# Kernel tuning notes

Measured on AMD Instinct MI355X. Metric: run time of the kernel, lower is better.

Reference implementation:

```python
import jax, jax.numpy as jnp
import numpy as np


def _pano_affinity():
    # Faithful port of get_pano_affinity(): 3 rings of 12 views, 3x3 Gaussian
    # blur (cv2 ksize=3 sigma=0 => sigma=0.8), BORDER_TRANSPARENT (borders kept),
    # diagonal reset to 1; zeros replaced by 0.01 as done in __init__.
    p = np.eye(36, dtype=np.float64)
    for v in range(12):  # top ring
        p[v, v + 12] = 1
        l = (v - 1) % 12
        r = (v + 1) % 12
        p[v, l] = 1; p[v, l + 12] = 1
        p[v, r] = 1; p[v, r + 12] = 1
    for v in range(12, 24):  # middle ring
        p[v, v + 12] = 1; p[v, v - 12] = 1
        l = (v - 13) % 12 + 12
        r = (v - 11) % 12 + 12
        p[v, l] = 1; p[v, l + 12] = 1; p[v, l - 12] = 1
        p[v, r] = 1; p[v, r + 12] = 1; p[v, r - 12] = 1
    for v in range(24, 36):  # bottom ring
        p[v, v - 12] = 1
        l = (v - 25) % 12 + 24
        r = (v - 23) % 12 + 24
        p[v, l] = 1; p[v, l - 12] = 1
        p[v, r] = 1; p[v, r - 12] = 1
    assert np.sum(p - p.T) == 0
    kern = np.exp(-np.array([-1.0, 0.0, 1.0]) ** 2 / (2 * 0.8 ** 2))
    kern /= kern.sum()
    a, b = kern[0], kern[1]
    t = a * p[:, :-2] + b * p[:, 1:-1] + a * p[:, 2:]
    t2 = a * t[:-2, :] + b * t[1:-1, :] + a * t[2:, :]
    out = p.copy()
    out[1:-1, 1:-1] = t2  # transparent border: edge pixels unblurred
    out[np.eye(36, dtype=bool)] = 1.0
    out[out == 0] = 0.01
    return out.astype(np.float32)


def _ln(x, g, b):
    mu = jnp.mean(x, -1, keepdims=True)
    v = jnp.mean(jnp.square(x - mu), -1, keepdims=True)
    return (x - mu) * jax.lax.rsqrt(v + 1e-5) * g + b


def setup_inputs() -> dict:
    key = jax.random.key(0)
    ks = jax.random.split(key, 12)
    B, L, V, D, KD, KV, Q, H = 128, 36, 36, 512, 300, 112, 36, 512
    s = 0.02
    return {
        'h': jax.random.normal(ks[0], (B, Q), jnp.float32),
        'context': jax.random.normal(ks[1], (B, L, V, D), jnp.float32),
        'teacher_action_view_ids': jax.random.randint(ks[2], (B,), 0, 36),
        'detect_feats': jax.random.normal(ks[3], (B, L, KD), jnp.float32),
        'knowledge_vector': jax.random.normal(ks[4], (B, L, KV), jnp.float32),
        'pano_a': jnp.asarray(_pano_affinity()),
        'W_q': jax.random.normal(ks[5], (Q, Q), jnp.float32) * s,
        'W_k': jax.random.normal(ks[6], (Q, D + KD), jnp.float32) * s,
        'gru_Wih': jax.random.normal(ks[7], (3 * Q, D + KV), jnp.float32) * s,
        'gru_Whh': jax.random.normal(ks[8], (3 * Q, Q), jnp.float32) * s,
        'gru_bih': jnp.zeros((3 * Q,), jnp.float32),
        'gru_bhh': jnp.zeros((3 * Q,), jnp.float32),
        'ln_slots_g': jnp.ones((Q,), jnp.float32),
        'ln_slots_b': jnp.zeros((Q,), jnp.float32),
        'ln_ff_g': jnp.ones((Q,), jnp.float32),
        'ln_ff_b': jnp.zeros((Q,), jnp.float32),
        'mlp_W1': jax.random.normal(ks[9], (H, Q), jnp.float32) * s,
        'mlp_b1': jnp.zeros((H,), jnp.float32),
        'mlp_W2': jax.random.normal(ks[10], (Q, H), jnp.float32) * s,
        'mlp_b2': jnp.zeros((Q,), jnp.float32),
    }


def reference(h, context, teacher_action_view_ids, detect_feats, knowledge_vector,
              pano_a, W_q, W_k, gru_Wih, gru_Whh, gru_bih, gru_bhh,
              ln_slots_g, ln_slots_b, ln_ff_g, ln_ff_b,
              mlp_W1, mlp_b1, mlp_W2, mlp_b2):
    B, L, V, D = context.shape
    Q = pano_a.shape[0]  # 36
    scale = Q ** -0.5
    iters = 3
    slots = jnp.broadcast_to(pano_a, (B, Q, Q))
    # context_know = cat(context, detect_feats broadcast over 36 views)
    ck = jnp.concatenate(
        [context, jnp.broadcast_to(detect_feats[:, :, None, :], (B, L, V, detect_feats.shape[-1]))], axis=-1)
    k = jnp.einsum('bljc,qc->bljq', ck, W_k)  # [B,L,36,Q]
    attn_ws = []
    for _ in range(iters):
        slots_prev = slots
        q = jnp.einsum('bie,qe->biq', _ln(slots, ln_slots_g, ln_slots_b), W_q)  # [B,Q,Q]
        dots = jnp.einsum('bid,bkjd->bkj', q, k) * scale  # i summed out, as in source
        attn = jax.nn.softmax(dots, axis=-1)  # softmax over views
        attn_ws.append(attn)
        updates = jnp.einsum('bkjd,bij->bid', context, attn)  # [B,L,D]
        x = jnp.concatenate([updates, knowledge_vector], axis=-1).reshape(-1, D + knowledge_vector.shape[-1])
        hp = slots_prev.reshape(-1, Q)
        # torch.nn.GRUCell (gate order r, z, n)
        gx = x @ gru_Wih.T + gru_bih
        gh = hp @ gru_Whh.T + gru_bhh
        xr, xz, xn = jnp.split(gx, 3, axis=-1)
        hr, hz, hn = jnp.split(gh, 3, axis=-1)
        r = jax.nn.sigmoid(xr + hr)
        z = jax.nn.sigmoid(xz + hz)
        n = jnp.tanh(xn + r * hn)
        gnew = ((1.0 - z) * n + z * hp).reshape(B, -1, Q)
        ff = _ln(gnew, ln_ff_g, ln_ff_b)
        gnew = gnew + (jax.nn.relu(ff @ mlp_W1.T + mlp_b1) @ mlp_W2.T + mlp_b2)
        slots = gnew
    return slots, jnp.stack(attn_ws, 0)
```

## Files before the change

### kernel.cpp

```cpp
#include <hip/hip_runtime.h>

namespace {
constexpr int Bc = 128, Lc = 36, Vc = 36, Dc = 512, KDc = 300, KVc = 112, Qc = 36, Hc = 512;
constexpr int ROWS = Bc * Lc * Vc;
constexpr int BLn  = Bc * Lc;
constexpr int SLOT = Bc * Qc * Qc;
constexpr float SCALE = 1.0f / 6.0f;
}

__device__ __forceinline__ float wave_sum(float v) {
  #pragma unroll
  for (int off = 32; off > 0; off >>= 1) v += __shfl_xor(v, off, 64);
  return v;
}
__device__ __forceinline__ float wave_max(float v) {
  #pragma unroll
  for (int off = 32; off > 0; off >>= 1) v = fmaxf(v, __shfl_xor(v, off, 64));
  return v;
}
__device__ __forceinline__ float sigmoidf_(float x) { return 1.f / (1.f + __expf(-x)); }

__global__ void init_slots_kernel(const float* __restrict__ pano, float* __restrict__ slots) {
  int idx = blockIdx.x * 256 + threadIdx.x;
  slots[idx] = pano[idx % (Qc * Qc)];
}

__global__ __launch_bounds__(256) void csum_kernel(const float* __restrict__ ctx, float* __restrict__ csum) {
  int tid = blockIdx.x * 256 + threadIdx.x;
  int b  = tid / (Vc * Dc);
  int jd = tid % (Vc * Dc);
  const float* p = ctx + (size_t)b * Lc * Vc * Dc + jd;
  float s = 0.f;
  #pragma unroll
  for (int l = 0; l < Lc; ++l) s += p[(size_t)l * (Vc * Dc)];
  csum[tid] = s;
}

__global__ void kd_kernel(const float* __restrict__ det, const float* __restrict__ Wk,
                          float* __restrict__ kd) {
  __shared__ float ds[KDc];
  int bl = blockIdx.x; int t = threadIdx.x;
  for (int c = t; c < KDc; c += 64) ds[c] = det[(size_t)bl * KDc + c];
  __syncthreads();
  if (t < Qc) {
    const float* w = Wk + (size_t)t * 812 + 512;
    float acc = 0.f;
    #pragma unroll 4
    for (int c = 0; c < KDc; ++c) acc = fmaf(ds[c], w[c], acc);
    kd[(size_t)bl * Qc + t] = acc;
  }
}

__global__ __launch_bounds__(256) void k_gemm(const float* __restrict__ A, const float* __restrict__ Wk,
                       const float* __restrict__ kd, float* __restrict__ kout) {
  __shared__ __align__(16) float As[32 * 260];
  __shared__ __align__(16) float Bs[32 * 48];
  int t = threadIdx.x;
  int rb = blockIdx.x * 256;
  int tr = t & 63, tc = t >> 6;
  float acc[4][9];
  #pragma unroll
  for (int i = 0; i < 4; ++i)
    #pragma unroll
    for (int c = 0; c < 9; ++c) acc[i][c] = 0.f;

  for (int d0 = 0; d0 < 512; d0 += 32) {
    #pragma unroll
    for (int jj = 0; jj < 8; ++jj) {
      int idx = t + jj * 256;
      int kkb = (idx & 7) * 4, r = idx >> 3;
      const float4 v = *(const float4*)(A + (size_t)(rb + r) * 512 + d0 + kkb);
      As[(kkb + 0) * 260 + r] = v.x;
      As[(kkb + 1) * 260 + r] = v.y;
      As[(kkb + 2) * 260 + r] = v.z;
      As[(kkb + 3) * 260 + r] = v.w;
    }
    for (int idx = t; idx < 32 * 36; idx += 256) {
      int kk = idx / 36, c = idx % 36;
      Bs[kk * 48 + (c / 9) * 12 + (c % 9)] = Wk[(size_t)c * 812 + d0 + kk];
    }
    __syncthreads();
    #pragma unroll
    for (int kk = 0; kk < 32; ++kk) {
      const float4 a  = *(const float4*)&As[kk * 260 + tr * 4];
      const float* bp = &Bs[kk * 48 + tc * 12];
      const float4 b0 = *(const float4*)bp;
      const float4 b1 = *(const float4*)(bp + 4);
      const float  b8 = bp[8];
      const float av[4] = {a.x, a.y, a.z, a.w};
      const float bv[9] = {b0.x, b0.y, b0.z, b0.w, b1.x, b1.y, b1.z, b1.w, b8};
      #pragma unroll
      for (int i = 0; i < 4; ++i)
        #pragma unroll
        for (int c = 0; c < 9; ++c) acc[i][c] = fmaf(av[i], bv[c], acc[i][c]);
    }
    __syncthreads();
  }
  #pragma unroll
  for (int i = 0; i < 4; ++i) {
    int row = rb + tr * 4 + i;
    int bl = row / 36;
    #pragma unroll
    for (int c = 0; c < 9; ++c) {
      int q = tc * 9 + c;
      kout[(size_t)row * 36 + q] = acc[i][c] + kd[(size_t)bl * 36 + q];
    }
  }
}

__global__ __launch_bounds__(256) void prew_gemm(const float* __restrict__ A, int lda, int K, int k0,
                                                 const float* __restrict__ Wih, float* __restrict__ outp) {
  __shared__ __align__(16) float As[16 * 68];
  __shared__ __align__(16) float Bs[16 * 112];
  int t = threadIdx.x;
  int rb = blockIdx.x * 64;
  int tr = t & 63, tc = t >> 6;
  float acc[27];
  #pragma unroll
  for (int c = 0; c < 27; ++c) acc[c] = 0.f;

  for (int kk0 = 0; kk0 < K; kk0 += 16) {
    {
      int r = t >> 2, kq = (t & 3) * 4;
      const float4 v = *(const float4*)(A + (size_t)(rb + r) * lda + kk0 + kq);
      As[(kq + 0) * 68 + r] = v.x;
      As[(kq + 1) * 68 + r] = v.y;
      As[(kq + 2) * 68 + r] = v.z;
      As[(kq + 3) * 68 + r] = v.w;
    }
    for (int idx = t; idx < 16 * 108; idx += 256) {
      int k = idx / 108, c = idx % 108;
      Bs[k * 112 + (c / 27) * 28 + (c % 27)] = Wih[(size_t)c * 624 + k0 + kk0 + k];
    }
    __syncthreads();
    #pragma unroll
    for (int k = 0; k < 16; ++k) {
      const float a = As[k * 68 + tr];
      const float* bp = &Bs[k * 112 + tc * 28];
      float bv[27];
      #pragma unroll
      for (int c4 = 0; c4 < 6; ++c4) {
        float4 b4 = *(const float4*)(bp + c4 * 4);
        bv[c4 * 4 + 0] = b4.x; bv[c4 * 4 + 1] = b4.y; bv[c4 * 4 + 2] = b4.z; bv[c4 * 4 + 3] = b4.w;
      }
      bv[24] = bp[24]; bv[25] = bp[25]; bv[26] = bp[26];
      #pragma unroll
      for (int c = 0; c < 27; ++c) acc[c] = fmaf(a, bv[c], acc[c]);
    }
    __syncthreads();
  }
  int row = rb + tr;
  #pragma unroll
  for (int c = 0; c < 27; ++c)
    outp[(size_t)row * 108 + tc * 27 + c] = acc[c];
}

__global__ void lnqsum_kernel(const float* __restrict__ slots, const float* __restrict__ Wq,
                              const float* __restrict__ g, const float* __restrict__ bb,
                              float* __restrict__ qsum) {
  int b = blockIdx.x, lane = threadIdx.x;
  __shared__ float ls[Qc];
  float gv = 0.f, bv = 0.f;
  if (lane < Qc) { gv = g[lane]; bv = bb[lane]; }
  float lnsum = 0.f;
  for (int i = 0; i < Qc; ++i) {
    float x = (lane < Qc) ? slots[((size_t)b * Qc + i) * Qc + lane] : 0.f;
    float mu = wave_sum(x) * (1.f / 36.f);
    float d = x - mu;
    float var = wave_sum((lane < Qc) ? d * d : 0.f) * (1.f / 36.f);
    float ln = d * rsqrtf(var + 1e-5f) * gv + bv;
    if (lane < Qc) lnsum += ln;
  }
  if (lane < Qc) ls[lane] = lnsum;
  __syncthreads();
  if (lane < Qc) {
    float acc = 0.f;
    #pragma unroll
    for (int e = 0; e < Qc; ++e) acc = fmaf(ls[e], Wq[lane * Qc + e], acc);
    qsum[(size_t)b * Qc + lane] = acc;
  }
}

__global__ void dots_kernel(const float* __restrict__ kmat, const float* __restrict__ qsum,
                            float* __restrict__ attn_out) {
  int bl = blockIdx.x;
  int b = bl / Lc;
  int lane = threadIdx.x;
  __shared__ float qs[Qc];
  if (lane < Qc) qs[lane] = qsum[(size_t)b * Qc + lane];
  __syncthreads();
  float dot = 0.f;
  if (lane < Vc) {
    const float* kp = kmat + ((size_t)bl * Vc + lane) * Qc;
    #pragma unroll
    for (int c = 0; c < 9; ++c) {
      float4 kv = *(const float4*)(kp + c * 4);
      dot += kv.x * qs[4 * c] + kv.y * qs[4 * c + 1] + kv.z * qs[4 * c + 2] + kv.w * qs[4 * c + 3];
    }
  }
  dot *= SCALE;
  float m = wave_max((lane < Vc) ? dot : -1e30f);
  float e = (lane < Vc) ? __expf(dot - m) : 0.f;
  float s = wave_sum(e);
  if (lane < Vc) attn_out[(size_t)bl * Vc + lane] = e / s;
}

__global__ __launch_bounds__(128) void gxmix_kernel(const float* __restrict__ attn, const float* __restrict__ cw,
                             const float* __restrict__ gknw, float* __restrict__ gx) {
  int b = blockIdx.x;
  int c = threadIdx.x;
  __shared__ float at[Qc * Vc];
  for (int idx = threadIdx.x; idx < Qc * Vc; idx += 128) at[idx] = attn[(size_t)b * Qc * Vc + idx];
  __syncthreads();
  if (c >= 108) return;
  float cwv[36];
  #pragma unroll
  for (int j = 0; j < 36; ++j) cwv[j] = cw[((size_t)b * 36 + j) * 108 + c];
  #pragma unroll 2
  for (int i = 0; i < 36; ++i) {
    float acc = gknw[((size_t)b * 36 + i) * 108 + c];
    #pragma unroll
    for (int j = 0; j < 36; ++j) acc = fmaf(at[i * 36 + j], cwv[j], acc);
    gx[((size_t)b * 36 + i) * 108 + c] = acc;
  }
}

__global__ void gate_kernel(const float* __restrict__ slots, const float* __restrict__ gx,
                            const float* __restrict__ Whh, const float* __restrict__ bih,
                            const float* __restrict__ bhh, const float* __restrict__ lng,
                            const float* __restrict__ lnb, const float* __restrict__ b2,
                            float* __restrict__ ff, float* __restrict__ snew) {
  int row = blockIdx.x, lane = threadIdx.x;
  __shared__ float hps[Qc];
  float hp = 0.f;
  if (lane < Qc) { hp = slots[(size_t)row * Qc + lane]; hps[lane] = hp; }
  __syncthreads();
  float hprime = 0.f;
  if (lane < Qc) {
    float hr = bhh[lane], hz = bhh[36 + lane], hn = bhh[72 + lane];
    #pragma unroll 4
    for (int e = 0; e < Qc; ++e) {
      float h = hps[e];
      hr = fmaf(h, Whh[lane * 36 + e], hr);
      hz = fmaf(h, Whh[(36 + lane) * 36 + e], hz);
      hn = fmaf(h, Whh[(72 + lane) * 36 + e], hn);
    }
    float xr = gx[(size_t)row * 108 + lane]      + bih[lane];
    float xz = gx[(size_t)row * 108 + 36 + lane] + bih[36 + lane];
    float xn = gx[(size_t)row * 108 + 72 + lane] + bih[72 + lane];
    float r = sigmoidf_(xr + hr);
    float z = sigmoidf_(xz + hz);
    float n = tanhf(xn + r * hn);
    hprime = (1.f - z) * n + z * hp;
  }
  float mu = wave_sum((lane < Qc) ? hprime : 0.f) * (1.f / 36.f);
  float dd = hprime - mu;
  float var = wave_sum((lane < Qc) ? dd * dd : 0.f) * (1.f / 36.f);
  float rstd = rsqrtf(var + 1e-5f);
  if (lane < Qc) {
    ff[(size_t)row * Qc + lane]   = dd * rstd * lng[lane] + lnb[lane];
    snew[(size_t)row * Qc + lane] = hprime + b2[lane];
  }
}

__global__ __launch_bounds__(256) void mlp1_kernel(const float* __restrict__ ff, const float* __restrict__ W1,
                         const float* __restrict__ b1, float* __restrict__ mid) {
  __shared__ __align__(16) float As[36 * 68];
  __shared__ __align__(16) float Bs[36 * 132];
  int t = threadIdx.x;
  int mt = blockIdx.x % 72, nt = blockIdx.x / 72;
  int rb = mt * 64, cb = nt * 128;
  for (int idx = t; idx < 64 * 36; idx += 256) {
    int r = idx / 36, e = idx % 36;
    As[e * 68 + r] = ff[(size_t)(rb + r) * 36 + e];
  }
  for (int idx = t; idx < 128 * 36; idx += 256) {
    int c = idx / 36, e = idx % 36;
    Bs[e * 132 + c] = W1[(size_t)(cb + c) * 36 + e];
  }
  __syncthreads();
  int tr = t & 31, tc = t >> 5;
  float acc[2][16];
  #pragma unroll
  for (int ri = 0; ri < 2; ++ri)
    #pragma unroll
    for (int c = 0; c < 16; ++c) acc[ri][c] = 0.f;
  #pragma unroll 4
  for (int e = 0; e < 36; ++e) {
    const float2 a = *(const float2*)&As[e * 68 + tr * 2];
    const float* bp = &Bs[e * 132 + tc * 16];
    float bv[16];
    #pragma unroll
    for (int c4 = 0; c4 < 4; ++c4) {
      float4 b4 = *(const float4*)(bp + c4 * 4);
      bv[c4 * 4 + 0] = b4.x; bv[c4 * 4 + 1] = b4.y; bv[c4 * 4 + 2] = b4.z; bv[c4 * 4 + 3] = b4.w;
    }
    #pragma unroll
    for (int c = 0; c < 16; ++c) {
      acc[0][c] = fmaf(a.x, bv[c], acc[0][c]);
      acc[1][c] = fmaf(a.y, bv[c], acc[1][c]);
    }
  }
  #pragma unroll
  for (int ri = 0; ri < 2; ++ri) {
    int row = rb + tr * 2 + ri;
    #pragma unroll
    for (int c4 = 0; c4 < 4; ++c4) {
      int c0 = cb + tc * 16 + c4 * 4;
      float4 o;
      o.x = fmaxf(acc[ri][c4 * 4 + 0] + b1[c0 + 0], 0.f);
      o.y = fmaxf(acc[ri][c4 * 4 + 1] + b1[c0 + 1], 0.f);
      o.z = fmaxf(acc[ri][c4 * 4 + 2] + b1[c0 + 2], 0.f);
      o.w = fmaxf(acc[ri][c4 * 4 + 3] + b1[c0 + 3], 0.f);
      *(float4*)&mid[(size_t)row * 512 + c0] = o;
    }
  }
}

__global__ __launch_bounds__(256) void mlp2_kernel(const float* __restrict__ mid, const float* __restrict__ W2,
                         float* __restrict__ snew) {
  __shared__ __align__(16) float As[32 * 68];
  __shared__ __align__(16) float Bs[32 * 48];
  int t = threadIdx.x;
  int rb = blockIdx.x * 64;
  int tr = t & 63, tc = t >> 6;
  float acc[9];
  #pragma unroll
  for (int c = 0; c < 9; ++c) acc[c] = 0.f;
  for (int d0 = 0; d0 < 512; d0 += 32) {
    #pragma unroll
    for (int jj = 0; jj < 2; ++jj) {
      int idx = t + jj * 256;
      int kkb = (idx & 7) * 4, r = idx >> 3;
      const float4 v = *(const float4*)(mid + (size_t)(rb + r) * 512 + d0 + kkb);
      As[(kkb + 0) * 68 + r] = v.x;
      As[(kkb + 1) * 68 + r] = v.y;
      As[(kkb + 2) * 68 + r] = v.z;
      As[(kkb + 3) * 68 + r] = v.w;
    }
    for (int idx = t; idx < 36 * 32; idx += 256) {
      int kk = idx / 36, c = idx % 36;
      Bs[kk * 48 + (c / 9) * 12 + (c % 9)] = W2[(size_t)c * 512 + d0 + kk];
    }
    __syncthreads();
    #pragma unroll
    for (int kk = 0; kk < 32; ++kk) {
      const float a = As[kk * 68 + tr];
      const float* bp = &Bs[kk * 48 + tc * 12];
      const float4 b0 = *(const float4*)bp;
      const float4 b1 = *(const float4*)(bp + 4);
      const float  b8 = bp[8];
      const float bv[9] = {b0.x, b0.y, b0.z, b0.w, b1.x, b1.y, b1.z, b1.w, b8};
      #pragma unroll
      for (int c = 0; c < 9; ++c) acc[c] = fmaf(a, bv[c], acc[c]);
    }
    __syncthreads();
  }
  int row = rb + tr;
  #pragma unroll
  for (int c = 0; c < 9; ++c) {
    size_t o = (size_t)row * 36 + tc * 9 + c;
    snew[o] = snew[o] + acc[c];
  }
}

__global__ void copy_kernel(const float* __restrict__ src, float* __restrict__ dst) {
  int idx = blockIdx.x * 256 + threadIdx.x;
  dst[idx] = src[idx];
}

extern "C" void kernel_launch(void* const* d_in, const int* in_sizes, int n_in,
                              void* d_out, int out_size, void* d_ws, size_t ws_size,
                              hipStream_t stream) {
  const float* ctx  = (const float*)d_in[1];
  const float* det  = (const float*)d_in[3];
  const float* knw  = (const float*)d_in[4];
  const float* pano = (const float*)d_in[5];
  const float* Wq   = (const float*)d_in[6];
  const float* Wk   = (const float*)d_in[7];
  const float* Wih  = (const float*)d_in[8];
  const float* Whh  = (const float*)d_in[9];
  const float* bih  = (const float*)d_in[10];
  const float* bhh  = (const float*)d_in[11];
  const float* lsg  = (const float*)d_in[12];
  const float* lsb  = (const float*)d_in[13];
  const float* lfg  = (const float*)d_in[14];
  const float* lfb  = (const float*)d_in[15];
  const float* W1   = (const float*)d_in[16];
  const float* b1   = (const float*)d_in[17];
  const float* W2   = (const float*)d_in[18];
  const float* b2   = (const float*)d_in[19];
  float* out = (float*)d_out;

  float* w = (float*)d_ws;
  float* kmat   = w; w += (size_t)ROWS * 36;
  float* csum   = w; w += (size_t)Bc * Vc * Dc;
  float* mid    = csum;
  float* kd     = w; w += (size_t)BLn * Qc;
  float* slotsA = w; w += SLOT;
  float* slotsB = w; w += SLOT;
  float* qsum   = w; w += Bc * Qc;
  float* cw     = w; w += (size_t)BLn * 108;
  float* gknw   = w; w += (size_t)BLn * 108;
  float* gx     = w; w += (size_t)BLn * 108;
  float* ffb    = w; w += SLOT;

  float* cur = slotsA;
  float* nxt = slotsB;

  init_slots_kernel<<<648, 256, 0, stream>>>(pano, cur);
  csum_kernel<<<(Bc * Vc * Dc) / 256, 256, 0, stream>>>(ctx, csum);
  kd_kernel<<<BLn, 64, 0, stream>>>(det, Wk, kd);
  k_gemm<<<ROWS / 256, 256, 0, stream>>>(ctx, Wk, kd, kmat);
  prew_gemm<<<72, 256, 0, stream>>>(csum, 512, 512, 0,   Wih, cw);
  prew_gemm<<<72, 256, 0, stream>>>(knw,  112, 112, 512, Wih, gknw);

  for (int it = 0; it < 3; ++it) {
    float* attn = out + SLOT + (size_t)it * SLOT;
    lnqsum_kernel<<<Bc, 64, 0, stream>>>(cur, Wq, lsg, lsb, qsum);
    dots_kernel<<<BLn, 64, 0, stream>>>(kmat, qsum, attn);
    gxmix_kernel<<<Bc, 128, 0, stream>>>(attn, cw, gknw, gx);
    gate_kernel<<<BLn, 64, 0, stream>>>(cur, gx, Whh, bih, bhh, lfg, lfb, b2, ffb, nxt);
    mlp1_kernel<<<72 * 4, 256, 0, stream>>>(ffb, W1, b1, mid);
    mlp2_kernel<<<72, 256, 0, stream>>>(mid, W2, nxt);
    float* tmp = cur; cur = nxt; nxt = tmp;
  }
  copy_kernel<<<SLOT / 256, 256, 0, stream>>>(cur, out);
}
```

Measured before the change: 1.163 ms.

## Fuse recurrent slot-attention iterations into one per-batch persistent kernel

```diff
diff --git a/kernel.cpp b/kernel.cpp
--- a/kernel.cpp
+++ b/kernel.cpp
@@ -19,11 +19,6 @@
   return v;
 }
 __device__ __forceinline__ float sigmoidf_(float x) { return 1.f / (1.f + __expf(-x)); }
-
-__global__ void init_slots_kernel(const float* __restrict__ pano, float* __restrict__ slots) {
-  int idx = blockIdx.x * 256 + threadIdx.x;
-  slots[idx] = pano[idx % (Qc * Qc)];
-}
 
 __global__ __launch_bounds__(256) void csum_kernel(const float* __restrict__ ctx, float* __restrict__ csum) {
   int tid = blockIdx.x * 256 + threadIdx.x;
@@ -155,218 +150,182 @@
     outp[(size_t)row * 108 + tc * 27 + c] = acc[c];
 }
 
-__global__ void lnqsum_kernel(const float* __restrict__ slots, const float* __restrict__ Wq,
-                              const float* __restrict__ g, const float* __restrict__ bb,
-                              float* __restrict__ qsum) {
-  int b = blockIdx.x, lane = threadIdx.x;
-  __shared__ float ls[Qc];
-  float gv = 0.f, bv = 0.f;
-  if (lane < Qc) { gv = g[lane]; bv = bb[lane]; }
-  float lnsum = 0.f;
-  for (int i = 0; i < Qc; ++i) {
-    float x = (lane < Qc) ? slots[((size_t)b * Qc + i) * Qc + lane] : 0.f;
-    float mu = wave_sum(x) * (1.f / 36.f);
-    float d = x - mu;
-    float var = wave_sum((lane < Qc) ? d * d : 0.f) * (1.f / 36.f);
-    float ln = d * rsqrtf(var + 1e-5f) * gv + bv;
-    if (lane < Qc) lnsum += ln;
-  }
-  if (lane < Qc) ls[lane] = lnsum;
+__global__ __launch_bounds__(256) void mega_kernel(
+    const float* __restrict__ pano, const float* __restrict__ kmat,
+    const float* __restrict__ cw,   const float* __restrict__ gknw,
+    const float* __restrict__ Wq,   const float* __restrict__ Whh,
+    const float* __restrict__ bih,  const float* __restrict__ bhh,
+    const float* __restrict__ lsg,  const float* __restrict__ lsb,
+    const float* __restrict__ lfg,  const float* __restrict__ lfb,
+    const float* __restrict__ W1,   const float* __restrict__ b1,
+    const float* __restrict__ W2,   const float* __restrict__ b2,
+    float* __restrict__ out) {
+  const int b = blockIdx.x;
+  const int t = threadIdx.x;
+  const int wv = t >> 6, lane = t & 63;
+
+  __shared__ float s0[36 * 37], s1[36 * 37];
+  __shared__ float at[36 * 36];
+  __shared__ float cw_s[36 * 108], gk_s[36 * 108];
+  __shared__ float whh_s[108 * 37];
+  __shared__ float ff_s[36 * 37];
+  __shared__ float ls4[192];
+  __shared__ float qs[36];
+  __shared__ __align__(16) float wst[128 * 37];
+  __shared__ __align__(16) float mid_s[36 * 132];
+
+  for (int idx = t; idx < 1296; idx += 256) s0[(idx / 36) * 37 + idx % 36] = pano[idx];
+  for (int idx = t; idx < 3888; idx += 256) {
+    cw_s[idx] = cw[(size_t)b * 3888 + idx];
+    gk_s[idx] = gknw[(size_t)b * 3888 + idx];
+    whh_s[(idx / 36) * 37 + idx % 36] = Whh[idx];
+  }
+  float gv = 0.f, bv = 0.f, fg = 0.f, fb = 0.f, b2v = 0.f;
+  if (lane < 36) { gv = lsg[lane]; bv = lsb[lane]; fg = lfg[lane]; fb = lfb[lane]; b2v = b2[lane]; }
+  const float* kb = kmat + (size_t)b * 1296 * 36;
   __syncthreads();
-  if (lane < Qc) {
-    float acc = 0.f;
-    #pragma unroll
-    for (int e = 0; e < Qc; ++e) acc = fmaf(ls[e], Wq[lane * Qc + e], acc);
-    qsum[(size_t)b * Qc + lane] = acc;
-  }
-}
-
-__global__ void dots_kernel(const float* __restrict__ kmat, const float* __restrict__ qsum,
-                            float* __restrict__ attn_out) {
-  int bl = blockIdx.x;
-  int b = bl / Lc;
-  int lane = threadIdx.x;
-  __shared__ float qs[Qc];
-  if (lane < Qc) qs[lane] = qsum[(size_t)b * Qc + lane];
-  __syncthreads();
-  float dot = 0.f;
-  if (lane < Vc) {
-    const float* kp = kmat + ((size_t)bl * Vc + lane) * Qc;
-    #pragma unroll
-    for (int c = 0; c < 9; ++c) {
-      float4 kv = *(const float4*)(kp + c * 4);
-      dot += kv.x * qs[4 * c] + kv.y * qs[4 * c + 1] + kv.z * qs[4 * c + 2] + kv.w * qs[4 * c + 3];
-    }
-  }
-  dot *= SCALE;
-  float m = wave_max((lane < Vc) ? dot : -1e30f);
-  float e = (lane < Vc) ? __expf(dot - m) : 0.f;
-  float s = wave_sum(e);
-  if (lane < Vc) attn_out[(size_t)bl * Vc + lane] = e / s;
-}
-
-__global__ __launch_bounds__(128) void gxmix_kernel(const float* __restrict__ attn, const float* __restrict__ cw,
-                             const float* __restrict__ gknw, float* __restrict__ gx) {
-  int b = blockIdx.x;
-  int c = threadIdx.x;
-  __shared__ float at[Qc * Vc];
-  for (int idx = threadIdx.x; idx < Qc * Vc; idx += 128) at[idx] = attn[(size_t)b * Qc * Vc + idx];
-  __syncthreads();
-  if (c >= 108) return;
-  float cwv[36];
-  #pragma unroll
-  for (int j = 0; j < 36; ++j) cwv[j] = cw[((size_t)b * 36 + j) * 108 + c];
-  #pragma unroll 2
-  for (int i = 0; i < 36; ++i) {
-    float acc = gknw[((size_t)b * 36 + i) * 108 + c];
-    #pragma unroll
-    for (int j = 0; j < 36; ++j) acc = fmaf(at[i * 36 + j], cwv[j], acc);
-    gx[((size_t)b * 36 + i) * 108 + c] = acc;
-  }
-}
-
-__global__ void gate_kernel(const float* __restrict__ slots, const float* __restrict__ gx,
-                            const float* __restrict__ Whh, const float* __restrict__ bih,
-                            const float* __restrict__ bhh, const float* __restrict__ lng,
-                            const float* __restrict__ lnb, const float* __restrict__ b2,
-                            float* __restrict__ ff, float* __restrict__ snew) {
-  int row = blockIdx.x, lane = threadIdx.x;
-  __shared__ float hps[Qc];
-  float hp = 0.f;
-  if (lane < Qc) { hp = slots[(size_t)row * Qc + lane]; hps[lane] = hp; }
-  __syncthreads();
-  float hprime = 0.f;
-  if (lane < Qc) {
-    float hr = bhh[lane], hz = bhh[36 + lane], hn = bhh[72 + lane];
-    #pragma unroll 4
-    for (int e = 0; e < Qc; ++e) {
-      float h = hps[e];
-      hr = fmaf(h, Whh[lane * 36 + e], hr);
-      hz = fmaf(h, Whh[(36 + lane) * 36 + e], hz);
-      hn = fmaf(h, Whh[(72 + lane) * 36 + e], hn);
-    }
-    float xr = gx[(size_t)row * 108 + lane]      + bih[lane];
-    float xz = gx[(size_t)row * 108 + 36 + lane] + bih[36 + lane];
-    float xn = gx[(size_t)row * 108 + 72 + lane] + bih[72 + lane];
-    float r = sigmoidf_(xr + hr);
-    float z = sigmoidf_(xz + hz);
-    float n = tanhf(xn + r * hn);
-    hprime = (1.f - z) * n + z * hp;
-  }
-  float mu = wave_sum((lane < Qc) ? hprime : 0.f) * (1.f / 36.f);
-  float dd = hprime - mu;
-  float var = wave_sum((lane < Qc) ? dd * dd : 0.f) * (1.f / 36.f);
-  float rstd = rsqrtf(var + 1e-5f);
-  if (lane < Qc) {
-    ff[(size_t)row * Qc + lane]   = dd * rstd * lng[lane] + lnb[lane];
-    snew[(size_t)row * Qc + lane] = hprime + b2[lane];
-  }
-}
-
-__global__ __launch_bounds__(256) void mlp1_kernel(const float* __restrict__ ff, const float* __restrict__ W1,
-                         const float* __restrict__ b1, float* __restrict__ mid) {
-  __shared__ __align__(16) float As[36 * 68];
-  __shared__ __align__(16) float Bs[36 * 132];
-  int t = threadIdx.x;
-  int mt = blockIdx.x % 72, nt = blockIdx.x / 72;
-  int rb = mt * 64, cb = nt * 128;
-  for (int idx = t; idx < 64 * 36; idx += 256) {
-    int r = idx / 36, e = idx % 36;
-    As[e * 68 + r] = ff[(size_t)(rb + r) * 36 + e];
-  }
-  for (int idx = t; idx < 128 * 36; idx += 256) {
-    int c = idx / 36, e = idx % 36;
-    Bs[e * 132 + c] = W1[(size_t)(cb + c) * 36 + e];
-  }
-  __syncthreads();
-  int tr = t & 31, tc = t >> 5;
-  float acc[2][16];
-  #pragma unroll
-  for (int ri = 0; ri < 2; ++ri)
-    #pragma unroll
-    for (int c = 0; c < 16; ++c) acc[ri][c] = 0.f;
-  #pragma unroll 4
-  for (int e = 0; e < 36; ++e) {
-    const float2 a = *(const float2*)&As[e * 68 + tr * 2];
-    const float* bp = &Bs[e * 132 + tc * 16];
-    float bv[16];
-    #pragma unroll
-    for (int c4 = 0; c4 < 4; ++c4) {
-      float4 b4 = *(const float4*)(bp + c4 * 4);
-      bv[c4 * 4 + 0] = b4.x; bv[c4 * 4 + 1] = b4.y; bv[c4 * 4 + 2] = b4.z; bv[c4 * 4 + 3] = b4.w;
-    }
-    #pragma unroll
-    for (int c = 0; c < 16; ++c) {
-      acc[0][c] = fmaf(a.x, bv[c], acc[0][c]);
-      acc[1][c] = fmaf(a.y, bv[c], acc[1][c]);
-    }
-  }
-  #pragma unroll
-  for (int ri = 0; ri < 2; ++ri) {
-    int row = rb + tr * 2 + ri;
-    #pragma unroll
-    for (int c4 = 0; c4 < 4; ++c4) {
-      int c0 = cb + tc * 16 + c4 * 4;
-      float4 o;
-      o.x = fmaxf(acc[ri][c4 * 4 + 0] + b1[c0 + 0], 0.f);
-      o.y = fmaxf(acc[ri][c4 * 4 + 1] + b1[c0 + 1], 0.f);
-      o.z = fmaxf(acc[ri][c4 * 4 + 2] + b1[c0 + 2], 0.f);
-      o.w = fmaxf(acc[ri][c4 * 4 + 3] + b1[c0 + 3], 0.f);
-      *(float4*)&mid[(size_t)row * 512 + c0] = o;
-    }
-  }
-}
-
-__global__ __launch_bounds__(256) void mlp2_kernel(const float* __restrict__ mid, const float* __restrict__ W2,
-                         float* __restrict__ snew) {
-  __shared__ __align__(16) float As[32 * 68];
-  __shared__ __align__(16) float Bs[32 * 48];
-  int t = threadIdx.x;
-  int rb = blockIdx.x * 64;
-  int tr = t & 63, tc = t >> 6;
-  float acc[9];
-  #pragma unroll
-  for (int c = 0; c < 9; ++c) acc[c] = 0.f;
-  for (int d0 = 0; d0 < 512; d0 += 32) {
-    #pragma unroll
-    for (int jj = 0; jj < 2; ++jj) {
-      int idx = t + jj * 256;
-      int kkb = (idx & 7) * 4, r = idx >> 3;
-      const float4 v = *(const float4*)(mid + (size_t)(rb + r) * 512 + d0 + kkb);
-      As[(kkb + 0) * 68 + r] = v.x;
-      As[(kkb + 1) * 68 + r] = v.y;
-      As[(kkb + 2) * 68 + r] = v.z;
-      As[(kkb + 3) * 68 + r] = v.w;
-    }
-    for (int idx = t; idx < 36 * 32; idx += 256) {
-      int kk = idx / 36, c = idx % 36;
-      Bs[kk * 48 + (c / 9) * 12 + (c % 9)] = W2[(size_t)c * 512 + d0 + kk];
-    }
-    __syncthreads();
-    #pragma unroll
-    for (int kk = 0; kk < 32; ++kk) {
-      const float a = As[kk * 68 + tr];
-      const float* bp = &Bs[kk * 48 + tc * 12];
-      const float4 b0 = *(const float4*)bp;
-      const float4 b1 = *(const float4*)(bp + 4);
-      const float  b8 = bp[8];
-      const float bv[9] = {b0.x, b0.y, b0.z, b0.w, b1.x, b1.y, b1.z, b1.w, b8};
-      #pragma unroll
-      for (int c = 0; c < 9; ++c) acc[c] = fmaf(a, bv[c], acc[c]);
-    }
-    __syncthreads();
-  }
-  int row = rb + tr;
-  #pragma unroll
-  for (int c = 0; c < 9; ++c) {
-    size_t o = (size_t)row * 36 + tc * 9 + c;
-    snew[o] = snew[o] + acc[c];
-  }
-}
-
-__global__ void copy_kernel(const float* __restrict__ src, float* __restrict__ dst) {
-  int idx = blockIdx.x * 256 + threadIdx.x;
-  dst[idx] = src[idx];
+
+  #pragma unroll
+  for (int it = 0; it < 3; ++it) {
+    float* cur = (it == 1) ? s1 : s0;
+    float* nxt = (it == 1) ? s0 : s1;
+    float* aout = out + SLOT + (size_t)it * SLOT + (size_t)b * 1296;
+
+    float lnsum = 0.f;
+    #pragma unroll
+    for (int ii = 0; ii < 9; ++ii) {
+      int i = wv + 4 * ii;
+      float x = (lane < 36) ? cur[i * 37 + lane] : 0.f;
+      float mu = wave_sum(x) * (1.f / 36.f);
+      float d = x - mu;
+      float var = wave_sum((lane < 36) ? d * d : 0.f) * (1.f / 36.f);
+      float ln = d * rsqrtf(var + 1e-5f) * gv + bv;
+      if (lane < 36) lnsum += ln;
+    }
+    if (lane < 36) ls4[wv * 37 + lane] = lnsum;
+    __syncthreads();
+    if (t < 36) {
+      float l0 = ls4[t] + ls4[37 + t] + ls4[74 + t] + ls4[111 + t];
+      ls4[148 + t] = l0;
+    }
+    if (t < 36) {
+      float acc = 0.f;
+      #pragma unroll
+      for (int e = 0; e < 36; ++e) acc = fmaf(ls4[148 + e], Wq[t * 36 + e], acc);
+      qs[t] = acc;
+    }
+    __syncthreads();
+
+    #pragma unroll
+    for (int ii = 0; ii < 9; ++ii) {
+      int l = wv * 9 + ii;
+      float dot = 0.f;
+      if (lane < 36) {
+        const float* kp = kb + ((size_t)l * 36 + lane) * 36;
+        #pragma unroll
+        for (int c = 0; c < 9; ++c) {
+          float4 kv = *(const float4*)(kp + 4 * c);
+          dot += kv.x * qs[4 * c] + kv.y * qs[4 * c + 1] + kv.z * qs[4 * c + 2] + kv.w * qs[4 * c + 3];
+        }
+      }
+      dot *= SCALE;
+      float m = wave_max((lane < 36) ? dot : -1e30f);
+      float e = (lane < 36) ? __expf(dot - m) : 0.f;
+      float s = wave_sum(e);
+      if (lane < 36) {
+        float a = e / s;
+        at[l * 36 + lane] = a;
+        aout[(size_t)l * 36 + lane] = a;
+      }
+    }
+    __syncthreads();
+
+    for (int idx = t; idx < 1296; idx += 256) {
+      int i = idx / 36, c = idx % 36;
+      const float* ar = &at[i * 36];
+      float xr = gk_s[i * 108 + c]      + bih[c];
+      float xz = gk_s[i * 108 + 36 + c] + bih[36 + c];
+      float xn = gk_s[i * 108 + 72 + c] + bih[72 + c];
+      #pragma unroll 4
+      for (int j = 0; j < 36; ++j) {
+        float a = ar[j];
+        xr = fmaf(a, cw_s[j * 108 + c],      xr);
+        xz = fmaf(a, cw_s[j * 108 + 36 + c], xz);
+        xn = fmaf(a, cw_s[j * 108 + 72 + c], xn);
+      }
+      float hr = bhh[c], hz = bhh[36 + c], hn = bhh[72 + c];
+      const float* hrow = &cur[i * 37];
+      #pragma unroll 4
+      for (int e = 0; e < 36; ++e) {
+        float h = hrow[e];
+        hr = fmaf(h, whh_s[c * 37 + e],        hr);
+        hz = fmaf(h, whh_s[(36 + c) * 37 + e], hz);
+        hn = fmaf(h, whh_s[(72 + c) * 37 + e], hn);
+      }
+      float r = sigmoidf_(xr + hr), z = sigmoidf_(xz + hz);
+      float n = tanhf(xn + r * hn);
+      nxt[i * 37 + c] = (1.f - z) * n + z * hrow[c];
+    }
+    __syncthreads();
+
+    #pragma unroll
+    for (int ii = 0; ii < 9; ++ii) {
+      int i = wv * 9 + ii;
+      float v = (lane < 36) ? nxt[i * 37 + lane] : 0.f;
+      float mu = wave_sum(v) * (1.f / 36.f);
+      float d = v - mu;
+      float var = wave_sum((lane < 36) ? d * d : 0.f) * (1.f / 36.f);
+      float rstd = rsqrtf(var + 1e-5f);
+      if (lane < 36) {
+        ff_s[i * 37 + lane] = d * rstd * fg + fb;
+        nxt[i * 37 + lane] = v + b2v;
+      }
+    }
+    __syncthreads();
+
+    float acc[6] = {0.f, 0.f, 0.f, 0.f, 0.f, 0.f};
+    for (int h0 = 0; h0 < 512; h0 += 128) {
+      for (int idx = t; idx < 4608; idx += 256)
+        wst[(idx / 36) * 37 + idx % 36] = W1[(size_t)h0 * 36 + idx];
+      __syncthreads();
+      for (int idx = t; idx < 4608; idx += 256) {
+        int i = idx >> 7, hh = idx & 127;
+        float a = b1[h0 + hh];
+        const float* fr = &ff_s[i * 37];
+        const float* wr = &wst[hh * 37];
+        #pragma unroll 4
+        for (int e = 0; e < 36; ++e) a = fmaf(fr[e], wr[e], a);
+        mid_s[i * 132 + hh] = fmaxf(a, 0.f);
+      }
+      __syncthreads();
+      for (int idx = t; idx < 4608; idx += 256)
+        wst[(idx >> 7) * 129 + (idx & 127)] = W2[(size_t)(idx >> 7) * 512 + h0 + (idx & 127)];
+      __syncthreads();
+      #pragma unroll
+      for (int pi = 0; pi < 6; ++pi) {
+        int idx = t + pi * 256;
+        if (idx < 1296) {
+          int i = idx / 36, c = idx % 36;
+          const float* mr = &mid_s[i * 132];
+          const float* wr = &wst[c * 129];
+          float a = acc[pi];
+          #pragma unroll 4
+          for (int hh = 0; hh < 128; ++hh) a = fmaf(mr[hh], wr[hh], a);
+          acc[pi] = a;
+        }
+      }
+      __syncthreads();
+    }
+    #pragma unroll
+    for (int pi = 0; pi < 6; ++pi) {
+      int idx = t + pi * 256;
+      if (idx < 1296) nxt[(idx / 36) * 37 + idx % 36] += acc[pi];
+    }
+    __syncthreads();
+  }
+
+  for (int idx = t; idx < 1296; idx += 256)
+    out[(size_t)b * 1296 + idx] = s1[(idx / 36) * 37 + idx % 36];
 }
 
 extern "C" void kernel_launch(void* const* d_in, const int* in_sizes, int n_in,
@@ -393,37 +352,17 @@
   float* out = (float*)d_out;
 
   float* w = (float*)d_ws;
-  float* kmat   = w; w += (size_t)ROWS * 36;
-  float* csum   = w; w += (size_t)Bc * Vc * Dc;
-  float* mid    = csum;
-  float* kd     = w; w += (size_t)BLn * Qc;
-  float* slotsA = w; w += SLOT;
-  float* slotsB = w; w += SLOT;
-  float* qsum   = w; w += Bc * Qc;
-  float* cw     = w; w += (size_t)BLn * 108;
-  float* gknw   = w; w += (size_t)BLn * 108;
-  float* gx     = w; w += (size_t)BLn * 108;
-  float* ffb    = w; w += SLOT;
-
-  float* cur = slotsA;
-  float* nxt = slotsB;
-
-  init_slots_kernel<<<648, 256, 0, stream>>>(pano, cur);
+  float* kmat = w; w += (size_t)ROWS * 36;
+  float* csum = w; w += (size_t)Bc * Vc * Dc;
+  float* kd   = w; w += (size_t)BLn * Qc;
+  float* cw   = w; w += (size_t)BLn * 108;
+  float* gknw = w; w += (size_t)BLn * 108;
+
   csum_kernel<<<(Bc * Vc * Dc) / 256, 256, 0, stream>>>(ctx, csum);
   kd_kernel<<<BLn, 64, 0, stream>>>(det, Wk, kd);
   k_gemm<<<ROWS / 256, 256, 0, stream>>>(ctx, Wk, kd, kmat);
   prew_gemm<<<72, 256, 0, stream>>>(csum, 512, 512, 0,   Wih, cw);
   prew_gemm<<<72, 256, 0, stream>>>(knw,  112, 112, 512, Wih, gknw);
-
-  for (int it = 0; it < 3; ++it) {
-    float* attn = out + SLOT + (size_t)it * SLOT;
-    lnqsum_kernel<<<Bc, 64, 0, stream>>>(cur, Wq, lsg, lsb, qsum);
-    dots_kernel<<<BLn, 64, 0, stream>>>(kmat, qsum, attn);
-    gxmix_kernel<<<Bc, 128, 0, stream>>>(attn, cw, gknw, gx);
-    gate_kernel<<<BLn, 64, 0, stream>>>(cur, gx, Whh, bih, bhh, lfg, lfb, b2, ffb, nxt);
-    mlp1_kernel<<<72 * 4, 256, 0, stream>>>(ffb, W1, b1, mid);
-    mlp2_kernel<<<72, 256, 0, stream>>>(mid, W2, nxt);
-    float* tmp = cur; cur = nxt; nxt = tmp;
-  }
-  copy_kernel<<<SLOT / 256, 256, 0, stream>>>(cur, out);
-}
+  mega_kernel<<<Bc, 256, 0, stream>>>(pano, kmat, cw, gknw, Wq, Whh, bih, bhh,
+                                      lsg, lsb, lfg, lfb, W1, b1, W2, b2, out);
+}
```

Result: no change. 1.178 ms (+1.4%).
